# Optimization experiments

Measured on AMD Instinct MI355X. Metric: run time of the kernel, lower is better.

Reference implementation:

```python
import jax, jax.numpy as jnp
import numpy as np

B, S, HID = 1, 4096, 2048
H, KV, D = 16, 8, 128
EPS = 1e-6
ROPE_THETA = 10000.0


def _rms_norm(x, w, eps=EPS):
    # x: [..., D], normalize over last dim in fp32 like Qwen3 RMSNorm
    xf = x.astype(jnp.float32)
    var = jnp.mean(xf * xf, axis=-1, keepdims=True)
    return (xf * jax.lax.rsqrt(var + eps)).astype(x.dtype) * w


def _rotate_half(x):
    x1, x2 = jnp.split(x, 2, axis=-1)
    return jnp.concatenate([-x2, x1], axis=-1)


def setup_inputs() -> dict:
    key = jax.random.key(0)
    ks = jax.random.split(key, 6)
    hidden_states = jax.random.normal(ks[0], (B, S, HID), dtype=jnp.float32)
    wq = jax.random.normal(ks[1], (H * D, HID), dtype=jnp.float32) * 0.02
    wk = jax.random.normal(ks[2], (KV * D, HID), dtype=jnp.float32) * 0.02
    wv = jax.random.normal(ks[3], (KV * D, HID), dtype=jnp.float32) * 0.02
    wo = jax.random.normal(ks[4], (HID, H * D), dtype=jnp.float32) * 0.02
    q_norm_w = jnp.ones((D,), dtype=jnp.float32)
    k_norm_w = jnp.ones((D,), dtype=jnp.float32)
    # real rotary tables: inv_freq over half dim, duplicated (HF convention)
    inv_freq = 1.0 / (ROPE_THETA ** (jnp.arange(0, D, 2, dtype=jnp.float32) / D))
    pos = jnp.arange(S, dtype=jnp.float32)
    freqs = pos[:, None] * inv_freq[None, :]          # [S, D/2]
    emb = jnp.concatenate([freqs, freqs], axis=-1)    # [S, D]
    cos = jnp.cos(emb)[None].astype(jnp.float32)      # [B, S, D]
    sin = jnp.sin(emb)[None].astype(jnp.float32)
    return {"hidden_states": hidden_states, "cos": cos, "sin": sin,
            "wq": wq, "wk": wk, "wv": wv, "wo": wo,
            "q_norm_w": q_norm_w, "k_norm_w": k_norm_w}


def reference(hidden_states, cos, sin, wq, wk, wv, wo, q_norm_w, k_norm_w):
    b, s, _ = hidden_states.shape
    scaling = D ** -0.5
    # QKV projections (no bias), reshape to heads, QK RMSNorm, then [b, h, s, d]
    q = _rms_norm(jnp.einsum('bsh,oh->bso', hidden_states, wq).reshape(b, s, H, D), q_norm_w)
    k = _rms_norm(jnp.einsum('bsh,oh->bso', hidden_states, wk).reshape(b, s, KV, D), k_norm_w)
    v = jnp.einsum('bsh,oh->bso', hidden_states, wv).reshape(b, s, KV, D)
    q = q.transpose(0, 2, 1, 3)  # [b, H, s, d]
    k = k.transpose(0, 2, 1, 3)  # [b, KV, s, d]
    v = v.transpose(0, 2, 1, 3)
    # RoPE (cos/sin broadcast over head dim)
    c = cos[:, None, :, :]
    sn = sin[:, None, :, :]
    q = q * c + _rotate_half(q) * sn
    k = k * c + _rotate_half(k) * sn
    # GQA: repeat KV heads to H
    groups = H // KV
    k = jnp.repeat(k, groups, axis=1)
    v = jnp.repeat(v, groups, axis=1)
    # eager causal attention, softmax in fp32
    scores = jnp.einsum('bhqd,bhkd->bhqk', q, k) * scaling
    causal = jnp.tril(jnp.ones((s, s), dtype=bool))
    scores = jnp.where(causal[None, None], scores, jnp.finfo(jnp.float32).min)
    attn = jax.nn.softmax(scores.astype(jnp.float32), axis=-1).astype(q.dtype)
    out = jnp.einsum('bhqk,bhkd->bhqd', attn, v)
    out = out.transpose(0, 2, 1, 3).reshape(b, s, H * D)
    return jnp.einsum('bso,ho->bsh', out, wo)
```

## Files before the change

### kernel.cpp

```cpp
#include <hip/hip_runtime.h>
#include <hip/hip_bf16.h>

typedef __hip_bfloat16 bf16;
typedef __attribute__((ext_vector_type(8))) short short8;
typedef __attribute__((ext_vector_type(4))) float f32x4;

#define S_LEN 4096
#define HID_DIM 2048

#define QSCALE ((float)(0.08838834764831845 * 1.4426950408889634))

__device__ __forceinline__ void gld_lds16(const void* g, void* l) {
  __builtin_amdgcn_global_load_lds(
      (const __attribute__((address_space(1))) void*)g,
      (__attribute__((address_space(3))) void*)l, 16, 0, 0);
}

__device__ __forceinline__ float fexp2(float x) {
  return __builtin_amdgcn_exp2f(x);
}

__device__ __forceinline__ unsigned cvtpk_bf16(float lo, float hi) {
  unsigned r;
  asm("v_cvt_pk_bf16_f32 %0, %1, %2" : "=v"(r) : "v"(lo), "v"(hi));
  return r;
}

__global__ __launch_bounds__(256) void k_cvt(const float* __restrict__ src,
                                             bf16* __restrict__ dst, int n) {
  long i = ((long)blockIdx.x * 256 + threadIdx.x) * 8;
  if (i >= n) return;
  float4 a = *reinterpret_cast<const float4*>(src + i);
  float4 b = *reinterpret_cast<const float4*>(src + i + 4);
  float v[8] = {a.x, a.y, a.z, a.w, b.x, b.y, b.z, b.w};
  short8 o;
#pragma unroll
  for (int j = 0; j < 8; ++j) {
    bf16 h = __float2bfloat16(v[j]);
    o[j] = *reinterpret_cast<short*>(&h);
  }
  *reinterpret_cast<short8*>(dst + i) = o;
}

template <typename OutT>
__global__ __launch_bounds__(512, 1) void k_gemm256(
    const bf16* __restrict__ A, const bf16* __restrict__ B,
    OutT* __restrict__ C, int M, int N, int K) {
  __shared__ bf16 Al[2][256 * 64];
  __shared__ bf16 Bl[2][256 * 64];
  const int tid = threadIdx.x;
  const int lane = tid & 63;
  const int wid = tid >> 6;
  const int wr = wid >> 2;
  const int wc = wid & 3;
  const long brow = (long)blockIdx.y * 256;
  const long bcol = (long)blockIdx.x * 256;
  const int NT = K >> 6;

  auto stage = [&](int kt, int buf) {
    const bf16* At = A + brow * K + kt * 64;
    const bf16* Bt = B + bcol * K + kt * 64;
#pragma unroll
    for (int i = 0; i < 4; ++i) {
      const int ch = tid + i * 512;
      const int row = ch >> 3;
      const int j = (ch & 7) ^ (row & 7);
      gld_lds16(At + (size_t)row * K + j * 8, &Al[buf][(wid * 64 + i * 512) * 8]);
    }
#pragma unroll
    for (int i = 0; i < 4; ++i) {
      const int ch = tid + i * 512;
      const int row = ch >> 3;
      const int j = (ch & 7) ^ (row & 7);
      gld_lds16(Bt + (size_t)row * K + j * 8, &Bl[buf][(wid * 64 + i * 512) * 8]);
    }
  };

  f32x4 acc0[4][4], acc1[4][4];
#pragma unroll
  for (int m = 0; m < 4; ++m)
#pragma unroll
    for (int n = 0; n < 4; ++n) {
      acc0[m][n] = (f32x4){0.f, 0.f, 0.f, 0.f};
      acc1[m][n] = (f32x4){0.f, 0.f, 0.f, 0.f};
    }

  const int l15 = lane & 15;
  const int cp0 = ((lane >> 4) ^ (lane & 7)) * 8;
  const int cp1 = ((4 + (lane >> 4)) ^ (lane & 7)) * 8;

  stage(0, 0);
  stage(1, 1);
  asm volatile("s_waitcnt vmcnt(8)" ::: "memory");
  __builtin_amdgcn_s_barrier();

  for (int kt = 0; kt < NT; ++kt) {
    const bf16* Ab = &Al[kt & 1][0];
    const bf16* Bb = &Bl[kt & 1][0];
    short8 bB[4][2], aA[4][2];
#pragma unroll
    for (int n = 0; n < 4; ++n) {
      const int rb = (wc * 64 + n * 16 + l15) * 64;
      bB[n][0] = *reinterpret_cast<const short8*>(&Bb[rb + cp0]);
      bB[n][1] = *reinterpret_cast<const short8*>(&Bb[rb + cp1]);
    }
#pragma unroll
    for (int m = 0; m < 4; ++m) {
      const int ra = (wr * 128 + m * 16 + l15) * 64;
      aA[m][0] = *reinterpret_cast<const short8*>(&Ab[ra + cp0]);
      aA[m][1] = *reinterpret_cast<const short8*>(&Ab[ra + cp1]);
    }
    __builtin_amdgcn_s_setprio(1);
#pragma unroll
    for (int m = 0; m < 4; ++m)
#pragma unroll
      for (int n = 0; n < 4; ++n) {
        acc0[m][n] = __builtin_amdgcn_mfma_f32_16x16x32_bf16(aA[m][0], bB[n][0],
                                                             acc0[m][n], 0, 0, 0);
        acc0[m][n] = __builtin_amdgcn_mfma_f32_16x16x32_bf16(aA[m][1], bB[n][1],
                                                             acc0[m][n], 0, 0, 0);
      }
    __builtin_amdgcn_s_setprio(0);
#pragma unroll
    for (int m = 0; m < 4; ++m) {
      const int ra = (wr * 128 + 64 + m * 16 + l15) * 64;
      aA[m][0] = *reinterpret_cast<const short8*>(&Ab[ra + cp0]);
      aA[m][1] = *reinterpret_cast<const short8*>(&Ab[ra + cp1]);
    }
    __builtin_amdgcn_s_setprio(1);
#pragma unroll
    for (int m = 0; m < 4; ++m)
#pragma unroll
      for (int n = 0; n < 4; ++n) {
        acc1[m][n] = __builtin_amdgcn_mfma_f32_16x16x32_bf16(aA[m][0], bB[n][0],
                                                             acc1[m][n], 0, 0, 0);
        acc1[m][n] = __builtin_amdgcn_mfma_f32_16x16x32_bf16(aA[m][1], bB[n][1],
                                                             acc1[m][n], 0, 0, 0);
      }
    __builtin_amdgcn_s_setprio(0);

    if (kt + 1 < NT) {
      __builtin_amdgcn_s_barrier();
      if (kt + 2 < NT) {
        stage(kt + 2, kt & 1);
        asm volatile("s_waitcnt vmcnt(8)" ::: "memory");
      } else {
        asm volatile("s_waitcnt vmcnt(0)" ::: "memory");
      }
      __builtin_amdgcn_s_barrier();
    }
  }

#pragma unroll
  for (int mh = 0; mh < 2; ++mh) {
#pragma unroll
    for (int m = 0; m < 4; ++m) {
      const long r0 = brow + wr * 128 + mh * 64 + m * 16 + (lane >> 4) * 4;
#pragma unroll
      for (int n = 0; n < 4; ++n) {
        const long c0 = bcol + wc * 64 + n * 16 + l15;
        const f32x4 v = mh ? acc1[m][n] : acc0[m][n];
#pragma unroll
        for (int r = 0; r < 4; ++r) {
          if constexpr (sizeof(OutT) == 2)
            C[(r0 + r) * N + c0] = __float2bfloat16(v[r]);
          else
            C[(r0 + r) * N + c0] = v[r];
        }
      }
    }
  }
}

template <typename OutT>
__global__ __launch_bounds__(256) void k_gemm_bt(
    const bf16* __restrict__ A, const bf16* __restrict__ B,
    OutT* __restrict__ C, int M, int N, int K) {
  __shared__ bf16 Al[2][128 * 32];
  __shared__ bf16 Bl[2][128 * 32];
  const int tid = threadIdx.x;
  const int lane = tid & 63;
  const int wid = tid >> 6;
  const int wr = wid >> 1;
  const int wc = wid & 1;
  const long brow = (long)blockIdx.y * 128;
  const long bcol = (long)blockIdx.x * 128;
  const int rsub = lane >> 2;
  const int ksub = (lane & 3) * 8;

  f32x4 acc[4][4];
#pragma unroll
  for (int i = 0; i < 4; ++i)
#pragma unroll
    for (int j = 0; j < 4; ++j) acc[i][j] = (f32x4){0.f, 0.f, 0.f, 0.f};

  const int NT = K >> 5;

  auto stage = [&](int buf, int kt) {
    const long k0 = (long)kt << 5;
#pragma unroll
    for (int ci = 0; ci < 2; ++ci) {
      const int c = wid + ci * 4;
      gld_lds16(A + (brow + c * 16 + rsub) * K + k0 + ksub, &Al[buf][c * 512]);
      gld_lds16(B + (bcol + c * 16 + rsub) * K + k0 + ksub, &Bl[buf][c * 512]);
    }
  };

  stage(0, 0);
  __syncthreads();

  const int arow = wr * 64 + (lane & 15);
  const int nrow = wc * 64 + (lane & 15);
  const int kk = (lane >> 4) * 8;

  for (int t = 0; t < NT; ++t) {
    const int buf = t & 1;
    if (t + 1 < NT) stage(buf ^ 1, t + 1);
    short8 af[4], bfr[4];
#pragma unroll
    for (int mt = 0; mt < 4; ++mt)
      af[mt] = *reinterpret_cast<const short8*>(&Al[buf][(arow + mt * 16) * 32 + kk]);
#pragma unroll
    for (int nt = 0; nt < 4; ++nt)
      bfr[nt] = *reinterpret_cast<const short8*>(&Bl[buf][(nrow + nt * 16) * 32 + kk]);
#pragma unroll
    for (int mt = 0; mt < 4; ++mt)
#pragma unroll
      for (int nt = 0; nt < 4; ++nt)
        acc[mt][nt] = __builtin_amdgcn_mfma_f32_16x16x32_bf16(af[mt], bfr[nt],
                                                              acc[mt][nt], 0, 0, 0);
    __syncthreads();
  }

#pragma unroll
  for (int mt = 0; mt < 4; ++mt) {
    const long r0 = brow + wr * 64 + mt * 16 + (lane >> 4) * 4;
#pragma unroll
    for (int nt = 0; nt < 4; ++nt) {
      const long c0 = bcol + wc * 64 + nt * 16 + (lane & 15);
#pragma unroll
      for (int r = 0; r < 4; ++r) {
        if constexpr (sizeof(OutT) == 2)
          C[(r0 + r) * N + c0] = __float2bfloat16(acc[mt][nt][r]);
        else
          C[(r0 + r) * N + c0] = acc[mt][nt][r];
      }
    }
  }
}

__global__ __launch_bounds__(256) void k_normrope(
    const bf16* __restrict__ QKVb, const float* __restrict__ cosb,
    const float* __restrict__ sinb, const float* __restrict__ qw,
    const float* __restrict__ kw, bf16* __restrict__ Qb, bf16* __restrict__ Kb,
    bf16* __restrict__ Vb) {
  const int lane = threadIdx.x & 63;
  const int row = blockIdx.x * 4 + (threadIdx.x >> 6);
  const int s = row >> 5;
  const int idx = row & 31;
  const bf16* src = QKVb + (size_t)s * 4096 + idx * 128;
  float x0 = __bfloat162float(src[lane]);
  float x1 = __bfloat162float(src[lane + 64]);
  if (idx < 24) {
    float ss = x0 * x0 + x1 * x1;
#pragma unroll
    for (int off = 1; off < 64; off <<= 1) ss += __shfl_xor(ss, off);
    const float rn = rsqrtf(ss * (1.f / 128.f) + 1e-6f);
    const float* w = (idx < 16) ? qw : kw;
    x0 = x0 * rn * w[lane];
    x1 = x1 * rn * w[lane + 64];
    const float c0 = cosb[(size_t)s * 128 + lane];
    const float c1 = cosb[(size_t)s * 128 + lane + 64];
    const float s0 = sinb[(size_t)s * 128 + lane];
    const float s1 = sinb[(size_t)s * 128 + lane + 64];
    float o0 = x0 * c0 - x1 * s0;
    float o1 = x1 * c1 + x0 * s1;
    if (idx < 16) { o0 *= QSCALE; o1 *= QSCALE; }
    bf16* dst = (idx < 16) ? (Qb + ((size_t)idx * S_LEN + s) * 128)
                           : (Kb + ((size_t)(idx - 16) * S_LEN + s) * 128);
    dst[lane] = __float2bfloat16(o0);
    dst[lane + 64] = __float2bfloat16(o1);
  } else {
    bf16* dst = Vb + ((size_t)(idx - 24) * S_LEN + s) * 128;
    dst[lane] = __float2bfloat16(x0);
    dst[lane + 64] = __float2bfloat16(x1);
  }
}

__global__ __launch_bounds__(256) void k_vt(const bf16* __restrict__ Vb,
                                            bf16* __restrict__ Vt) {
  __shared__ bf16 Lds[64][136];
  const int tid = threadIdx.x;
  const int s0 = blockIdx.x * 64;
  const int kv = blockIdx.y;
#pragma unroll
  for (int pass = 0; pass < 4; ++pass) {
    const int c = tid + pass * 256;
    const int r = c >> 4;
    const int off = (c & 15) * 8;
    *reinterpret_cast<short8*>(&Lds[r][off]) =
        *reinterpret_cast<const short8*>(
            &Vb[((size_t)kv * S_LEN + s0 + r) * 128 + off]);
  }
  __syncthreads();
#pragma unroll
  for (int pass = 0; pass < 4; ++pass) {
    const int c = tid + pass * 256;
    const int d = c >> 3;
    const int so = (c & 7) * 8;
    short8 o;
#pragma unroll
    for (int j = 0; j < 8; ++j) {
      bf16 e = Lds[so + j][d];
      o[j] = *reinterpret_cast<short*>(&e);
    }
    *reinterpret_cast<short8*>(&Vt[((size_t)kv * 128 + d) * S_LEN + s0 + so]) = o;
  }
}

__global__ __launch_bounds__(256) void k_attn(const bf16* __restrict__ Qb,
                                              const bf16* __restrict__ Kb,
                                              const bf16* __restrict__ Vt_g,
                                              bf16* __restrict__ AO) {
  __shared__ bf16 Kl[2][64 * 128];
  __shared__ bf16 Vl[2][128 * 64];
  __shared__ bf16 Pl[4][16 * 64];
  const int tid = threadIdx.x;
  const int lane = tid & 63;
  const int wv = tid >> 6;
  const int h = blockIdx.y;
  const int kvh = h >> 1;
  const int c16 = lane & 15;
  const int hi = lane >> 4;
  const int kk = hi * 8;

  const bf16* Kbase = Kb + (size_t)kvh * S_LEN * 128;
  const bf16* Vbase = Vt_g + (size_t)kvh * 128 * S_LEN;

  auto stage = [&](int t, int buf) {
    const bf16* Kt = Kbase + (size_t)t * 64 * 128;
    const bf16* Vt = Vbase + t * 64;
#pragma unroll
    for (int p = 0; p < 4; ++p) {
      const int ch = tid + p * 256;
      const int row = ch >> 4, cp = ch & 15;
      const int c = (cp & 8) | ((cp & 7) ^ (row & 7));
      gld_lds16(Kt + row * 128 + c * 8, &Kl[buf][(wv * 64 + p * 256) * 8]);
    }
#pragma unroll
    for (int p = 0; p < 4; ++p) {
      const int ch = tid + p * 256;
      const int d = ch >> 3, cp = ch & 7;
      const int c = cp ^ (d & 7);
      gld_lds16(Vt + (size_t)d * S_LEN + c * 8, &Vl[buf][(wv * 64 + p * 256) * 8]);
    }
  };

  for (int half = 0; half < 2; ++half) {
    const int qt = half ? (63 - blockIdx.x) : blockIdx.x;
    const int qrow = qt * 64 + wv * 16;
    const int grow = qrow + c16;

    __syncthreads();
    stage(0, 0);

    short8 qf[4];
    {
      const bf16* qp = Qb + ((size_t)h * S_LEN + qrow + c16) * 128 + kk;
#pragma unroll
      for (int ks = 0; ks < 4; ++ks)
        qf[ks] = *reinterpret_cast<const short8*>(qp + ks * 32);
    }

    f32x4 oacc[8];
#pragma unroll
    for (int i = 0; i < 8; ++i) oacc[i] = (f32x4){0.f, 0.f, 0.f, 0.f};
    float m_run = -1e30f;
    float l_part = 0.f;

    auto tile = [&](int t, int buf, bool mask) {
      f32x4 sacc[4];
#pragma unroll
      for (int nt = 0; nt < 4; ++nt) sacc[nt] = (f32x4){0.f, 0.f, 0.f, 0.f};
#pragma unroll
      for (int ks = 0; ks < 4; ++ks) {
#pragma unroll
        for (int nt = 0; nt < 4; ++nt) {
          const int row = nt * 16 + c16;
          const int ck = ks * 4 + hi;
          const int ckp = (ck & 8) | ((ck & 7) ^ (row & 7));
          short8 kf =
              *reinterpret_cast<const short8*>(&Kl[buf][row * 128 + ckp * 8]);
          sacc[nt] = __builtin_amdgcn_mfma_f32_16x16x32_bf16(kf, qf[ks],
                                                             sacc[nt], 0, 0, 0);
        }
      }

      float tm = -1e30f;
#pragma unroll
      for (int nt = 0; nt < 4; ++nt)
#pragma unroll
        for (int r = 0; r < 4; ++r) {
          float sv = sacc[nt][r];
          if (mask && (t * 64 + nt * 16 + 4 * hi + r > grow)) sv = -1e30f;
          sacc[nt][r] = sv;
          tm = fmaxf(tm, sv);
        }
      tm = fmaxf(tm, __shfl_xor(tm, 16));
      tm = fmaxf(tm, __shfl_xor(tm, 32));
      if (__any(tm > m_run + 8.f)) {
        const float mn = fmaxf(m_run, tm);
        const float alpha = fexp2(m_run - mn);
        m_run = mn;
        l_part *= alpha;
#pragma unroll
        for (int dn = 0; dn < 8; ++dn) oacc[dn] *= alpha;
      }

#pragma unroll
      for (int nt = 0; nt < 4; ++nt) {
        const float p0 = fexp2(sacc[nt][0] - m_run);
        const float p1 = fexp2(sacc[nt][1] - m_run);
        const float p2 = fexp2(sacc[nt][2] - m_run);
        const float p3 = fexp2(sacc[nt][3] - m_run);
        l_part += (p0 + p1) + (p2 + p3);
        const unsigned w0 = cvtpk_bf16(p0, p1);
        const unsigned w1 = cvtpk_bf16(p2, p3);
        const int chunk = (2 * nt + (hi >> 1)) ^ (c16 & 7);
        const int base = c16 * 64 + chunk * 8 + 4 * (hi & 1);
        *reinterpret_cast<unsigned*>(&Pl[wv][base]) = w0;
        *reinterpret_cast<unsigned*>(&Pl[wv][base + 2]) = w1;
      }

#pragma unroll
      for (int ks = 0; ks < 2; ++ks) {
        const int pc = (ks * 4 + hi) ^ (c16 & 7);
        short8 pf =
            *reinterpret_cast<const short8*>(&Pl[wv][c16 * 64 + pc * 8]);
#pragma unroll
        for (int dn = 0; dn < 8; ++dn) {
          const int d = dn * 16 + c16;
          const int cvp = (ks * 4 + hi) ^ (d & 7);
          short8 vf =
              *reinterpret_cast<const short8*>(&Vl[buf][d * 64 + cvp * 8]);
          oacc[dn] =
              __builtin_amdgcn_mfma_f32_16x16x32_bf16(vf, pf, oacc[dn], 0, 0, 0);
        }
      }
    };

    __syncthreads();
    int cur = 0;
    for (int t = 0; t < qt; ++t) {
      stage(t + 1, cur ^ 1);
      tile(t, cur, false);
      __syncthreads();
      cur ^= 1;
    }
    tile(qt, cur, true);

    float lt = l_part;
    lt += __shfl_xor(lt, 16);
    lt += __shfl_xor(lt, 32);
    const float inv = 1.f / lt;
    bf16* dst = AO + (size_t)grow * HID_DIM + h * 128;
#pragma unroll
    for (int dn = 0; dn < 8; ++dn) {
#pragma unroll
      for (int w = 0; w < 2; ++w) {
        const unsigned pk = cvtpk_bf16(oacc[dn][2 * w] * inv,
                                       oacc[dn][2 * w + 1] * inv);
        *reinterpret_cast<unsigned*>(&dst[dn * 16 + 4 * hi + 2 * w]) = pk;
      }
    }
  }
}

extern "C" void kernel_launch(void* const* d_in, const int* in_sizes, int n_in,
                              void* d_out, int out_size, void* d_ws,
                              size_t ws_size, hipStream_t stream) {
  (void)in_sizes; (void)n_in; (void)out_size; (void)ws_size;
  const float* hs = (const float*)d_in[0];
  const float* cosb = (const float*)d_in[1];
  const float* sinb = (const float*)d_in[2];
  const float* wq = (const float*)d_in[3];
  const float* wk = (const float*)d_in[4];
  const float* wv = (const float*)d_in[5];
  const float* wo = (const float*)d_in[6];
  const float* qnw = (const float*)d_in[7];
  const float* knw = (const float*)d_in[8];
  float* out = (float*)d_out;
  char* ws = (char*)d_ws;

  bf16* Ah = (bf16*)(ws + 0);
  bf16* Wqkv = (bf16*)(ws + 16777216);
  bf16* Wo = (bf16*)(ws + 33554432);
  bf16* QKVb = (bf16*)(ws + 41943040);
  bf16* Qb = (bf16*)(ws + 75497472);
  bf16* Kb = (bf16*)(ws + 92274688);
  bf16* Vb = (bf16*)(ws + 100663296);
  bf16* AO = (bf16*)(ws + 109051904);
  bf16* Vt = (bf16*)(ws + 125829120);

  auto cvt = [&](const float* s, bf16* d, long n) {
    k_cvt<<<dim3((unsigned)((n / 8 + 255) / 256)), dim3(256), 0, stream>>>(
        s, d, (int)n);
  };
  cvt(hs, Ah, (long)S_LEN * HID_DIM);
  cvt(wq, Wqkv, (long)2048 * 2048);
  cvt(wk, Wqkv + (long)2048 * 2048, (long)1024 * 2048);
  cvt(wv, Wqkv + (long)3072 * 2048, (long)1024 * 2048);
  cvt(wo, Wo, (long)2048 * 2048);

  k_gemm256<bf16><<<dim3(16, 16), dim3(512), 0, stream>>>(Ah, Wqkv, QKVb, 4096,
                                                          4096, 2048);
  k_normrope<<<dim3(32768), dim3(256), 0, stream>>>(QKVb, cosb, sinb, qnw, knw,
                                                    Qb, Kb, Vb);
  k_vt<<<dim3(64, 8), dim3(256), 0, stream>>>(Vb, Vt);
  k_attn<<<dim3(32, 16), dim3(256), 0, stream>>>(Qb, Kb, Vt, AO);
  k_gemm_bt<float><<<dim3(16, 32), dim3(256), 0, stream>>>(AO, Wo, out, 4096,
                                                           2048, 2048);
}
```

Baseline: 287.9 us.

## Split causal attention KV range across two blocks and merge fp32 partials

The attention kernel now has each wave handle two 16-row query groups (128 query rows per block), so every K/V fragment read from LDS feeds twice as many MFMAs. The causal KV range for each 128-row group is split between two blocks, keeping the same grid size with balanced work. Each block writes unnormalized fp32 output partials plus row max and sum to workspace, and a new merge kernel combines them into bf16. The trade-off is extra register pressure, an additional launch, and roughly 64MB of fp32 partials written and read back. Workspace buffers are re-laid out so the partials reuse regions freed by earlier stages.

```diff
diff --git a/kernel.cpp b/kernel.cpp
--- a/kernel.cpp
+++ b/kernel.cpp
@@ -318,18 +318,20 @@
   }
 }
 
-__global__ __launch_bounds__(256) void k_attn(const bf16* __restrict__ Qb,
-                                              const bf16* __restrict__ Kb,
-                                              const bf16* __restrict__ Vt_g,
-                                              bf16* __restrict__ AO) {
+__global__ __launch_bounds__(256) void k_attn_part(
+    const bf16* __restrict__ Qb, const bf16* __restrict__ Kb,
+    const bf16* __restrict__ Vt_g, float* __restrict__ Opart,
+    float* __restrict__ ML) {
   __shared__ bf16 Kl[2][64 * 128];
   __shared__ bf16 Vl[2][128 * 64];
-  __shared__ bf16 Pl[4][16 * 64];
+  __shared__ bf16 Pl[4][32 * 64];
   const int tid = threadIdx.x;
   const int lane = tid & 63;
   const int wv = tid >> 6;
   const int h = blockIdx.y;
   const int kvh = h >> 1;
+  const int pr = blockIdx.x >> 1;
+  const int part = blockIdx.x & 1;
   const int c16 = lane & 15;
   const int hi = lane >> 4;
   const int kk = hi * 8;
@@ -356,32 +358,48 @@
     }
   };
 
-  for (int half = 0; half < 2; ++half) {
-    const int qt = half ? (63 - blockIdx.x) : blockIdx.x;
-    const int qrow = qt * 64 + wv * 16;
-    const int grow = qrow + c16;
-
-    __syncthreads();
-    stage(0, 0);
-
-    short8 qf[4];
+  for (int hf = 0; hf < 2; ++hf) {
+    const int g = hf ? (31 - pr) : pr;
+    const int qrowA = g * 128 + wv * 16;
+    const int growA = qrowA + c16;
+    const int growB = growA + 64;
+    const int t0 = part ? (g + 1) : 0;
+    const int t1 = part ? (2 * g + 2) : (g + 1);
+    const int diagA = 2 * g;
+    const int diagB = 2 * g + 1;
+
+    if (hf) __syncthreads();
+    stage(t0, 0);
+
+    short8 qfA[4], qfB[4];
     {
-      const bf16* qp = Qb + ((size_t)h * S_LEN + qrow + c16) * 128 + kk;
-#pragma unroll
-      for (int ks = 0; ks < 4; ++ks)
-        qf[ks] = *reinterpret_cast<const short8*>(qp + ks * 32);
-    }
-
-    f32x4 oacc[8];
-#pragma unroll
-    for (int i = 0; i < 8; ++i) oacc[i] = (f32x4){0.f, 0.f, 0.f, 0.f};
-    float m_run = -1e30f;
-    float l_part = 0.f;
-
-    auto tile = [&](int t, int buf, bool mask) {
-      f32x4 sacc[4];
-#pragma unroll
-      for (int nt = 0; nt < 4; ++nt) sacc[nt] = (f32x4){0.f, 0.f, 0.f, 0.f};
+      const bf16* qpA = Qb + ((size_t)h * S_LEN + growA) * 128 + kk;
+      const bf16* qpB = Qb + ((size_t)h * S_LEN + growB) * 128 + kk;
+#pragma unroll
+      for (int ks = 0; ks < 4; ++ks) {
+        qfA[ks] = *reinterpret_cast<const short8*>(qpA + ks * 32);
+        qfB[ks] = *reinterpret_cast<const short8*>(qpB + ks * 32);
+      }
+    }
+
+    f32x4 oA[8], oB[8];
+#pragma unroll
+    for (int i = 0; i < 8; ++i) {
+      oA[i] = (f32x4){0.f, 0.f, 0.f, 0.f};
+      oB[i] = (f32x4){0.f, 0.f, 0.f, 0.f};
+    }
+    float mA = -1e30f, mB = -1e30f, lA = 0.f, lB = 0.f;
+
+    auto tile = [&](int t, int buf) {
+      const bool doA = (t <= diagA);
+      const bool mkA = (t == diagA);
+      const bool mkB = (t == diagB);
+      f32x4 sA[4], sB[4];
+#pragma unroll
+      for (int nt = 0; nt < 4; ++nt) {
+        sA[nt] = (f32x4){0.f, 0.f, 0.f, 0.f};
+        sB[nt] = (f32x4){0.f, 0.f, 0.f, 0.f};
+      }
 #pragma unroll
       for (int ks = 0; ks < 4; ++ks) {
 #pragma unroll
@@ -391,89 +409,169 @@
           const int ckp = (ck & 8) | ((ck & 7) ^ (row & 7));
           short8 kf =
               *reinterpret_cast<const short8*>(&Kl[buf][row * 128 + ckp * 8]);
-          sacc[nt] = __builtin_amdgcn_mfma_f32_16x16x32_bf16(kf, qf[ks],
-                                                             sacc[nt], 0, 0, 0);
+          if (doA)
+            sA[nt] = __builtin_amdgcn_mfma_f32_16x16x32_bf16(kf, qfA[ks],
+                                                             sA[nt], 0, 0, 0);
+          sB[nt] = __builtin_amdgcn_mfma_f32_16x16x32_bf16(kf, qfB[ks],
+                                                           sB[nt], 0, 0, 0);
         }
       }
 
-      float tm = -1e30f;
-#pragma unroll
-      for (int nt = 0; nt < 4; ++nt)
-#pragma unroll
-        for (int r = 0; r < 4; ++r) {
-          float sv = sacc[nt][r];
-          if (mask && (t * 64 + nt * 16 + 4 * hi + r > grow)) sv = -1e30f;
-          sacc[nt][r] = sv;
-          tm = fmaxf(tm, sv);
+      if (doA) {
+        float tm = -1e30f;
+#pragma unroll
+        for (int nt = 0; nt < 4; ++nt)
+#pragma unroll
+          for (int r = 0; r < 4; ++r) {
+            float sv = sA[nt][r];
+            if (mkA && (t * 64 + nt * 16 + 4 * hi + r > growA)) sv = -1e30f;
+            sA[nt][r] = sv;
+            tm = fmaxf(tm, sv);
+          }
+        tm = fmaxf(tm, __shfl_xor(tm, 16));
+        tm = fmaxf(tm, __shfl_xor(tm, 32));
+        if (__any(tm > mA + 8.f)) {
+          const float mn = fmaxf(mA, tm);
+          const float alpha = fexp2(mA - mn);
+          mA = mn;
+          lA *= alpha;
+#pragma unroll
+          for (int dn = 0; dn < 8; ++dn) oA[dn] *= alpha;
         }
-      tm = fmaxf(tm, __shfl_xor(tm, 16));
-      tm = fmaxf(tm, __shfl_xor(tm, 32));
-      if (__any(tm > m_run + 8.f)) {
-        const float mn = fmaxf(m_run, tm);
-        const float alpha = fexp2(m_run - mn);
-        m_run = mn;
-        l_part *= alpha;
-#pragma unroll
-        for (int dn = 0; dn < 8; ++dn) oacc[dn] *= alpha;
-      }
-
-#pragma unroll
-      for (int nt = 0; nt < 4; ++nt) {
-        const float p0 = fexp2(sacc[nt][0] - m_run);
-        const float p1 = fexp2(sacc[nt][1] - m_run);
-        const float p2 = fexp2(sacc[nt][2] - m_run);
-        const float p3 = fexp2(sacc[nt][3] - m_run);
-        l_part += (p0 + p1) + (p2 + p3);
-        const unsigned w0 = cvtpk_bf16(p0, p1);
-        const unsigned w1 = cvtpk_bf16(p2, p3);
-        const int chunk = (2 * nt + (hi >> 1)) ^ (c16 & 7);
-        const int base = c16 * 64 + chunk * 8 + 4 * (hi & 1);
-        *reinterpret_cast<unsigned*>(&Pl[wv][base]) = w0;
-        *reinterpret_cast<unsigned*>(&Pl[wv][base + 2]) = w1;
+#pragma unroll
+        for (int nt = 0; nt < 4; ++nt) {
+          const float p0 = fexp2(sA[nt][0] - mA);
+          const float p1 = fexp2(sA[nt][1] - mA);
+          const float p2 = fexp2(sA[nt][2] - mA);
+          const float p3 = fexp2(sA[nt][3] - mA);
+          lA += (p0 + p1) + (p2 + p3);
+          const unsigned w0 = cvtpk_bf16(p0, p1);
+          const unsigned w1 = cvtpk_bf16(p2, p3);
+          const int chunk = (2 * nt + (hi >> 1)) ^ (c16 & 7);
+          const int base = c16 * 64 + chunk * 8 + 4 * (hi & 1);
+          *reinterpret_cast<unsigned*>(&Pl[wv][base]) = w0;
+          *reinterpret_cast<unsigned*>(&Pl[wv][base + 2]) = w1;
+        }
+      }
+      {
+        float tm = -1e30f;
+#pragma unroll
+        for (int nt = 0; nt < 4; ++nt)
+#pragma unroll
+          for (int r = 0; r < 4; ++r) {
+            float sv = sB[nt][r];
+            if (mkB && (t * 64 + nt * 16 + 4 * hi + r > growB)) sv = -1e30f;
+            sB[nt][r] = sv;
+            tm = fmaxf(tm, sv);
+          }
+        tm = fmaxf(tm, __shfl_xor(tm, 16));
+        tm = fmaxf(tm, __shfl_xor(tm, 32));
+        if (__any(tm > mB + 8.f)) {
+          const float mn = fmaxf(mB, tm);
+          const float alpha = fexp2(mB - mn);
+          mB = mn;
+          lB *= alpha;
+#pragma unroll
+          for (int dn = 0; dn < 8; ++dn) oB[dn] *= alpha;
+        }
+#pragma unroll
+        for (int nt = 0; nt < 4; ++nt) {
+          const float p0 = fexp2(sB[nt][0] - mB);
+          const float p1 = fexp2(sB[nt][1] - mB);
+          const float p2 = fexp2(sB[nt][2] - mB);
+          const float p3 = fexp2(sB[nt][3] - mB);
+          lB += (p0 + p1) + (p2 + p3);
+          const unsigned w0 = cvtpk_bf16(p0, p1);
+          const unsigned w1 = cvtpk_bf16(p2, p3);
+          const int chunk = (2 * nt + (hi >> 1)) ^ (c16 & 7);
+          const int base = (16 + c16) * 64 + chunk * 8 + 4 * (hi & 1);
+          *reinterpret_cast<unsigned*>(&Pl[wv][base]) = w0;
+          *reinterpret_cast<unsigned*>(&Pl[wv][base + 2]) = w1;
+        }
       }
 
 #pragma unroll
       for (int ks = 0; ks < 2; ++ks) {
         const int pc = (ks * 4 + hi) ^ (c16 & 7);
-        short8 pf =
-            *reinterpret_cast<const short8*>(&Pl[wv][c16 * 64 + pc * 8]);
+        short8 pfA;
+        if (doA)
+          pfA = *reinterpret_cast<const short8*>(&Pl[wv][c16 * 64 + pc * 8]);
+        short8 pfB =
+            *reinterpret_cast<const short8*>(&Pl[wv][(16 + c16) * 64 + pc * 8]);
 #pragma unroll
         for (int dn = 0; dn < 8; ++dn) {
           const int d = dn * 16 + c16;
           const int cvp = (ks * 4 + hi) ^ (d & 7);
           short8 vf =
               *reinterpret_cast<const short8*>(&Vl[buf][d * 64 + cvp * 8]);
-          oacc[dn] =
-              __builtin_amdgcn_mfma_f32_16x16x32_bf16(vf, pf, oacc[dn], 0, 0, 0);
+          if (doA)
+            oA[dn] = __builtin_amdgcn_mfma_f32_16x16x32_bf16(vf, pfA, oA[dn],
+                                                             0, 0, 0);
+          oB[dn] = __builtin_amdgcn_mfma_f32_16x16x32_bf16(vf, pfB, oB[dn],
+                                                           0, 0, 0);
         }
       }
     };
 
     __syncthreads();
     int cur = 0;
-    for (int t = 0; t < qt; ++t) {
+    for (int t = t0; t < t1 - 1; ++t) {
       stage(t + 1, cur ^ 1);
-      tile(t, cur, false);
+      tile(t, cur);
       __syncthreads();
       cur ^= 1;
     }
-    tile(qt, cur, true);
-
-    float lt = l_part;
-    lt += __shfl_xor(lt, 16);
-    lt += __shfl_xor(lt, 32);
-    const float inv = 1.f / lt;
-    bf16* dst = AO + (size_t)grow * HID_DIM + h * 128;
+    tile(t1 - 1, cur);
+
+    float ltA = lA, ltB = lB;
+    ltA += __shfl_xor(ltA, 16);
+    ltA += __shfl_xor(ltA, 32);
+    ltB += __shfl_xor(ltB, 16);
+    ltB += __shfl_xor(ltB, 32);
+    const int job = (h * 32 + g) * 2 + part;
+    float* Op = Opart + (size_t)job * 128 * 128;
+    float* MLp = ML + (size_t)job * 256;
+    const int rA = wv * 16 + c16;
+    const int rB = rA + 64;
 #pragma unroll
     for (int dn = 0; dn < 8; ++dn) {
-#pragma unroll
-      for (int w = 0; w < 2; ++w) {
-        const unsigned pk = cvtpk_bf16(oacc[dn][2 * w] * inv,
-                                       oacc[dn][2 * w + 1] * inv);
-        *reinterpret_cast<unsigned*>(&dst[dn * 16 + 4 * hi + 2 * w]) = pk;
-      }
-    }
-  }
+      *reinterpret_cast<float4*>(&Op[rA * 128 + dn * 16 + 4 * hi]) =
+          *reinterpret_cast<float4*>(&oA[dn]);
+      *reinterpret_cast<float4*>(&Op[rB * 128 + dn * 16 + 4 * hi]) =
+          *reinterpret_cast<float4*>(&oB[dn]);
+    }
+    if (lane < 16) {
+      MLp[rA] = mA;
+      MLp[128 + rA] = ltA;
+      MLp[rB] = mB;
+      MLp[128 + rB] = ltB;
+    }
+  }
+}
+
+__global__ __launch_bounds__(256) void k_merge(const float* __restrict__ Opart,
+                                               const float* __restrict__ ML,
+                                               bf16* __restrict__ AO) {
+  const int idx = blockIdx.x * 4 + (threadIdx.x >> 6);
+  const int lane = threadIdx.x & 63;
+  const int h = idx >> 12;
+  const int s = idx & 4095;
+  const int g = s >> 7, rowin = s & 127;
+  const int j0 = (h * 32 + g) * 2;
+  const float m0 = ML[(size_t)j0 * 256 + rowin];
+  const float l0 = ML[(size_t)j0 * 256 + 128 + rowin];
+  const float m1 = ML[(size_t)(j0 + 1) * 256 + rowin];
+  const float l1 = ML[(size_t)(j0 + 1) * 256 + 128 + rowin];
+  const float mm = fmaxf(m0, m1);
+  const float a0 = fexp2(m0 - mm), a1 = fexp2(m1 - mm);
+  const float inv = 1.f / (l0 * a0 + l1 * a1);
+  const float2 o0 = *reinterpret_cast<const float2*>(
+      &Opart[((size_t)j0 * 128 + rowin) * 128 + lane * 2]);
+  const float2 o1 = *reinterpret_cast<const float2*>(
+      &Opart[((size_t)(j0 + 1) * 128 + rowin) * 128 + lane * 2]);
+  bf16* dst = AO + (size_t)s * HID_DIM + h * 128 + lane * 2;
+  dst[0] = __float2bfloat16((o0.x * a0 + o1.x * a1) * inv);
+  dst[1] = __float2bfloat16((o0.y * a0 + o1.y * a1) * inv);
 }
 
 extern "C" void kernel_launch(void* const* d_in, const int* in_sizes, int n_in,
@@ -494,13 +592,15 @@
 
   bf16* Ah = (bf16*)(ws + 0);
   bf16* Wqkv = (bf16*)(ws + 16777216);
-  bf16* Wo = (bf16*)(ws + 33554432);
-  bf16* QKVb = (bf16*)(ws + 41943040);
-  bf16* Qb = (bf16*)(ws + 75497472);
-  bf16* Kb = (bf16*)(ws + 92274688);
-  bf16* Vb = (bf16*)(ws + 100663296);
+  bf16* QKVb = (bf16*)(ws + 33554432);
+  bf16* Qb = (bf16*)(ws + 67108864);
+  bf16* Kb = (bf16*)(ws + 83886080);
+  bf16* Vb = (bf16*)(ws + 92274688);
+  bf16* Vt = (bf16*)(ws + 100663296);
   bf16* AO = (bf16*)(ws + 109051904);
-  bf16* Vt = (bf16*)(ws + 125829120);
+  bf16* Wo = (bf16*)(ws + 125829120);
+  float* Opart = (float*)(ws + 0);
+  float* ML = (float*)(ws + 92274688);
 
   auto cvt = [&](const float* s, bf16* d, long n) {
     k_cvt<<<dim3((unsigned)((n / 8 + 255) / 256)), dim3(256), 0, stream>>>(
@@ -517,7 +617,8 @@
   k_normrope<<<dim3(32768), dim3(256), 0, stream>>>(QKVb, cosb, sinb, qnw, knw,
                                                     Qb, Kb, Vb);
   k_vt<<<dim3(64, 8), dim3(256), 0, stream>>>(Vb, Vt);
-  k_attn<<<dim3(32, 16), dim3(256), 0, stream>>>(Qb, Kb, Vt, AO);
+  k_attn_part<<<dim3(32, 16), dim3(256), 0, stream>>>(Qb, Kb, Vt, Opart, ML);
+  k_merge<<<dim3(16384), dim3(256), 0, stream>>>(Opart, ML, AO);
   k_gemm_bt<float><<<dim3(16, 32), dim3(256), 0, stream>>>(AO, Wo, out, 4096,
                                                            2048, 2048);
 }
```

Result: slower. 383.8 us (+33.3%).

## Read V fragments directly from global in MFMA-ready layout, one q-tile per block

Applied to the files above, without the earlier changes.

The V transpose kernel now writes V in a chunked layout ([s/8][d][8]) so each lane's MFMA operand is one contiguous 16-byte global load. The attention kernel drops V staging in LDS and loads V fragments straight from global/L2, which halves the LDS footprint and the staging traffic. It also replaces the paired causal q-tile loop with one q-tile per block on a grid twice as large. The risks are global-load latency inside the inner PV loop, with no prefetch, and load imbalance now that heavy and light causal tiles are no longer paired per block.

```diff
diff --git a/kernel.cpp b/kernel.cpp
--- a/kernel.cpp
+++ b/kernel.cpp
@@ -288,7 +288,7 @@
 }
 
 __global__ __launch_bounds__(256) void k_vt(const bf16* __restrict__ Vb,
-                                            bf16* __restrict__ Vt) {
+                                            bf16* __restrict__ Vg) {
   __shared__ bf16 Lds[64][136];
   const int tid = threadIdx.x;
   const int s0 = blockIdx.x * 64;
@@ -306,24 +306,25 @@
 #pragma unroll
   for (int pass = 0; pass < 4; ++pass) {
     const int c = tid + pass * 256;
-    const int d = c >> 3;
-    const int so = (c & 7) * 8;
+    const int ck = c >> 7;
+    const int d = c & 127;
     short8 o;
 #pragma unroll
     for (int j = 0; j < 8; ++j) {
-      bf16 e = Lds[so + j][d];
+      bf16 e = Lds[ck * 8 + j][d];
       o[j] = *reinterpret_cast<short*>(&e);
     }
-    *reinterpret_cast<short8*>(&Vt[((size_t)kv * 128 + d) * S_LEN + s0 + so]) = o;
+    *reinterpret_cast<short8*>(
+        &Vg[(size_t)kv * S_LEN * 128 +
+            ((size_t)(blockIdx.x * 8 + ck) * 128 + d) * 8]) = o;
   }
 }
 
 __global__ __launch_bounds__(256) void k_attn(const bf16* __restrict__ Qb,
                                               const bf16* __restrict__ Kb,
-                                              const bf16* __restrict__ Vt_g,
+                                              const bf16* __restrict__ Vg,
                                               bf16* __restrict__ AO) {
   __shared__ bf16 Kl[2][64 * 128];
-  __shared__ bf16 Vl[2][128 * 64];
   __shared__ bf16 Pl[4][16 * 64];
   const int tid = threadIdx.x;
   const int lane = tid & 63;
@@ -335,11 +336,10 @@
   const int kk = hi * 8;
 
   const bf16* Kbase = Kb + (size_t)kvh * S_LEN * 128;
-  const bf16* Vbase = Vt_g + (size_t)kvh * 128 * S_LEN;
+  const bf16* Vgh = Vg + (size_t)kvh * S_LEN * 128;
 
   auto stage = [&](int t, int buf) {
     const bf16* Kt = Kbase + (size_t)t * 64 * 128;
-    const bf16* Vt = Vbase + t * 64;
 #pragma unroll
     for (int p = 0; p < 4; ++p) {
       const int ch = tid + p * 256;
@@ -347,131 +347,121 @@
       const int c = (cp & 8) | ((cp & 7) ^ (row & 7));
       gld_lds16(Kt + row * 128 + c * 8, &Kl[buf][(wv * 64 + p * 256) * 8]);
     }
-#pragma unroll
-    for (int p = 0; p < 4; ++p) {
-      const int ch = tid + p * 256;
-      const int d = ch >> 3, cp = ch & 7;
-      const int c = cp ^ (d & 7);
-      gld_lds16(Vt + (size_t)d * S_LEN + c * 8, &Vl[buf][(wv * 64 + p * 256) * 8]);
-    }
   };
 
-  for (int half = 0; half < 2; ++half) {
-    const int qt = half ? (63 - blockIdx.x) : blockIdx.x;
-    const int qrow = qt * 64 + wv * 16;
-    const int grow = qrow + c16;
-
+  const int qt = 63 - blockIdx.x;
+  const int qrow = qt * 64 + wv * 16;
+  const int grow = qrow + c16;
+
+  stage(0, 0);
+
+  short8 qf[4];
+  {
+    const bf16* qp = Qb + ((size_t)h * S_LEN + grow) * 128 + kk;
+#pragma unroll
+    for (int ks = 0; ks < 4; ++ks)
+      qf[ks] = *reinterpret_cast<const short8*>(qp + ks * 32);
+  }
+
+  f32x4 oacc[8];
+#pragma unroll
+  for (int i = 0; i < 8; ++i) oacc[i] = (f32x4){0.f, 0.f, 0.f, 0.f};
+  float m_run = -1e30f;
+  float l_part = 0.f;
+
+  auto tile = [&](int t, int buf, bool mask) {
+    f32x4 sacc[4];
+#pragma unroll
+    for (int nt = 0; nt < 4; ++nt) sacc[nt] = (f32x4){0.f, 0.f, 0.f, 0.f};
+#pragma unroll
+    for (int ks = 0; ks < 4; ++ks) {
+#pragma unroll
+      for (int nt = 0; nt < 4; ++nt) {
+        const int row = nt * 16 + c16;
+        const int ck = ks * 4 + hi;
+        const int ckp = (ck & 8) | ((ck & 7) ^ (row & 7));
+        short8 kf =
+            *reinterpret_cast<const short8*>(&Kl[buf][row * 128 + ckp * 8]);
+        sacc[nt] = __builtin_amdgcn_mfma_f32_16x16x32_bf16(kf, qf[ks],
+                                                           sacc[nt], 0, 0, 0);
+      }
+    }
+
+    float tm = -1e30f;
+#pragma unroll
+    for (int nt = 0; nt < 4; ++nt)
+#pragma unroll
+      for (int r = 0; r < 4; ++r) {
+        float sv = sacc[nt][r];
+        if (mask && (t * 64 + nt * 16 + 4 * hi + r > grow)) sv = -1e30f;
+        sacc[nt][r] = sv;
+        tm = fmaxf(tm, sv);
+      }
+    tm = fmaxf(tm, __shfl_xor(tm, 16));
+    tm = fmaxf(tm, __shfl_xor(tm, 32));
+    if (__any(tm > m_run + 8.f)) {
+      const float mn = fmaxf(m_run, tm);
+      const float alpha = fexp2(m_run - mn);
+      m_run = mn;
+      l_part *= alpha;
+#pragma unroll
+      for (int dn = 0; dn < 8; ++dn) oacc[dn] *= alpha;
+    }
+
+#pragma unroll
+    for (int nt = 0; nt < 4; ++nt) {
+      const float p0 = fexp2(sacc[nt][0] - m_run);
+      const float p1 = fexp2(sacc[nt][1] - m_run);
+      const float p2 = fexp2(sacc[nt][2] - m_run);
+      const float p3 = fexp2(sacc[nt][3] - m_run);
+      l_part += (p0 + p1) + (p2 + p3);
+      const unsigned w0 = cvtpk_bf16(p0, p1);
+      const unsigned w1 = cvtpk_bf16(p2, p3);
+      const int chunk = (2 * nt + (hi >> 1)) ^ (c16 & 7);
+      const int base = c16 * 64 + chunk * 8 + 4 * (hi & 1);
+      *reinterpret_cast<unsigned*>(&Pl[wv][base]) = w0;
+      *reinterpret_cast<unsigned*>(&Pl[wv][base + 2]) = w1;
+    }
+
+    const bf16* vt0 = Vgh + (size_t)t * 8192;
+#pragma unroll
+    for (int ks = 0; ks < 2; ++ks) {
+      const int pc = (ks * 4 + hi) ^ (c16 & 7);
+      short8 pf =
+          *reinterpret_cast<const short8*>(&Pl[wv][c16 * 64 + pc * 8]);
+      const bf16* vck = vt0 + (ks * 4 + hi) * 1024;
+#pragma unroll
+      for (int dn = 0; dn < 8; ++dn) {
+        short8 vf = *reinterpret_cast<const short8*>(
+            vck + (dn * 16 + c16) * 8);
+        oacc[dn] =
+            __builtin_amdgcn_mfma_f32_16x16x32_bf16(vf, pf, oacc[dn], 0, 0, 0);
+      }
+    }
+  };
+
+  __syncthreads();
+  int cur = 0;
+  for (int t = 0; t < qt; ++t) {
+    stage(t + 1, cur ^ 1);
+    tile(t, cur, false);
     __syncthreads();
-    stage(0, 0);
-
-    short8 qf[4];
-    {
-      const bf16* qp = Qb + ((size_t)h * S_LEN + qrow + c16) * 128 + kk;
-#pragma unroll
-      for (int ks = 0; ks < 4; ++ks)
-        qf[ks] = *reinterpret_cast<const short8*>(qp + ks * 32);
-    }
-
-    f32x4 oacc[8];
-#pragma unroll
-    for (int i = 0; i < 8; ++i) oacc[i] = (f32x4){0.f, 0.f, 0.f, 0.f};
-    float m_run = -1e30f;
-    float l_part = 0.f;
-
-    auto tile = [&](int t, int buf, bool mask) {
-      f32x4 sacc[4];
-#pragma unroll
-      for (int nt = 0; nt < 4; ++nt) sacc[nt] = (f32x4){0.f, 0.f, 0.f, 0.f};
-#pragma unroll
-      for (int ks = 0; ks < 4; ++ks) {
-#pragma unroll
-        for (int nt = 0; nt < 4; ++nt) {
-          const int row = nt * 16 + c16;
-          const int ck = ks * 4 + hi;
-          const int ckp = (ck & 8) | ((ck & 7) ^ (row & 7));
-          short8 kf =
-              *reinterpret_cast<const short8*>(&Kl[buf][row * 128 + ckp * 8]);
-          sacc[nt] = __builtin_amdgcn_mfma_f32_16x16x32_bf16(kf, qf[ks],
-                                                             sacc[nt], 0, 0, 0);
-        }
-      }
-
-      float tm = -1e30f;
-#pragma unroll
-      for (int nt = 0; nt < 4; ++nt)
-#pragma unroll
-        for (int r = 0; r < 4; ++r) {
-          float sv = sacc[nt][r];
-          if (mask && (t * 64 + nt * 16 + 4 * hi + r > grow)) sv = -1e30f;
-          sacc[nt][r] = sv;
-          tm = fmaxf(tm, sv);
-        }
-      tm = fmaxf(tm, __shfl_xor(tm, 16));
-      tm = fmaxf(tm, __shfl_xor(tm, 32));
-      if (__any(tm > m_run + 8.f)) {
-        const float mn = fmaxf(m_run, tm);
-        const float alpha = fexp2(m_run - mn);
-        m_run = mn;
-        l_part *= alpha;
-#pragma unroll
-        for (int dn = 0; dn < 8; ++dn) oacc[dn] *= alpha;
-      }
-
-#pragma unroll
-      for (int nt = 0; nt < 4; ++nt) {
-        const float p0 = fexp2(sacc[nt][0] - m_run);
-        const float p1 = fexp2(sacc[nt][1] - m_run);
-        const float p2 = fexp2(sacc[nt][2] - m_run);
-        const float p3 = fexp2(sacc[nt][3] - m_run);
-        l_part += (p0 + p1) + (p2 + p3);
-        const unsigned w0 = cvtpk_bf16(p0, p1);
-        const unsigned w1 = cvtpk_bf16(p2, p3);
-        const int chunk = (2 * nt + (hi >> 1)) ^ (c16 & 7);
-        const int base = c16 * 64 + chunk * 8 + 4 * (hi & 1);
-        *reinterpret_cast<unsigned*>(&Pl[wv][base]) = w0;
-        *reinterpret_cast<unsigned*>(&Pl[wv][base + 2]) = w1;
-      }
-
-#pragma unroll
-      for (int ks = 0; ks < 2; ++ks) {
-        const int pc = (ks * 4 + hi) ^ (c16 & 7);
-        short8 pf =
-            *reinterpret_cast<const short8*>(&Pl[wv][c16 * 64 + pc * 8]);
-#pragma unroll
-        for (int dn = 0; dn < 8; ++dn) {
-          const int d = dn * 16 + c16;
-          const int cvp = (ks * 4 + hi) ^ (d & 7);
-          short8 vf =
-              *reinterpret_cast<const short8*>(&Vl[buf][d * 64 + cvp * 8]);
-          oacc[dn] =
-              __builtin_amdgcn_mfma_f32_16x16x32_bf16(vf, pf, oacc[dn], 0, 0, 0);
-        }
-      }
-    };
-
-    __syncthreads();
-    int cur = 0;
-    for (int t = 0; t < qt; ++t) {
-      stage(t + 1, cur ^ 1);
-      tile(t, cur, false);
-      __syncthreads();
-      cur ^= 1;
-    }
-    tile(qt, cur, true);
-
-    float lt = l_part;
-    lt += __shfl_xor(lt, 16);
-    lt += __shfl_xor(lt, 32);
-    const float inv = 1.f / lt;
-    bf16* dst = AO + (size_t)grow * HID_DIM + h * 128;
-#pragma unroll
-    for (int dn = 0; dn < 8; ++dn) {
-#pragma unroll
-      for (int w = 0; w < 2; ++w) {
-        const unsigned pk = cvtpk_bf16(oacc[dn][2 * w] * inv,
-                                       oacc[dn][2 * w + 1] * inv);
-        *reinterpret_cast<unsigned*>(&dst[dn * 16 + 4 * hi + 2 * w]) = pk;
-      }
+    cur ^= 1;
+  }
+  tile(qt, cur, true);
+
+  float lt = l_part;
+  lt += __shfl_xor(lt, 16);
+  lt += __shfl_xor(lt, 32);
+  const float inv = 1.f / lt;
+  bf16* dst = AO + (size_t)grow * HID_DIM + h * 128;
+#pragma unroll
+  for (int dn = 0; dn < 8; ++dn) {
+#pragma unroll
+    for (int w = 0; w < 2; ++w) {
+      const unsigned pk = cvtpk_bf16(oacc[dn][2 * w] * inv,
+                                     oacc[dn][2 * w + 1] * inv);
+      *reinterpret_cast<unsigned*>(&dst[dn * 16 + 4 * hi + 2 * w]) = pk;
     }
   }
 }
@@ -500,7 +490,7 @@
   bf16* Kb = (bf16*)(ws + 92274688);
   bf16* Vb = (bf16*)(ws + 100663296);
   bf16* AO = (bf16*)(ws + 109051904);
-  bf16* Vt = (bf16*)(ws + 125829120);
+  bf16* Vg = (bf16*)(ws + 125829120);
 
   auto cvt = [&](const float* s, bf16* d, long n) {
     k_cvt<<<dim3((unsigned)((n / 8 + 255) / 256)), dim3(256), 0, stream>>>(
@@ -516,8 +506,8 @@
                                                           4096, 2048);
   k_normrope<<<dim3(32768), dim3(256), 0, stream>>>(QKVb, cosb, sinb, qnw, knw,
                                                     Qb, Kb, Vb);
-  k_vt<<<dim3(64, 8), dim3(256), 0, stream>>>(Vb, Vt);
-  k_attn<<<dim3(32, 16), dim3(256), 0, stream>>>(Qb, Kb, Vt, AO);
+  k_vt<<<dim3(64, 8), dim3(256), 0, stream>>>(Vb, Vg);
+  k_attn<<<dim3(64, 16), dim3(256), 0, stream>>>(Qb, Kb, Vg, AO);
   k_gemm_bt<float><<<dim3(16, 32), dim3(256), 0, stream>>>(AO, Wo, out, 4096,
                                                            2048, 2048);
 }
```

Measured after the change: 351.2 us. +22.0%, slower.

## Replace output-projection GEMM with 256x128 tile, BK=64, swizzled LDS pipeline

Applied to the files above, without the earlier changes.

The output projection GEMM moves from 128x128 tiles with K-step 32 and 256 threads to 256x128 tiles with K-step 64 and 512 threads. It adds XOR-swizzled LDS staging, prefetches two stages ahead with explicit vmcnt waits and raw barriers, and raises wave priority around the MFMA block. The aim is more data reuse per tile, fewer bank conflicts and better overlap of loads with compute. The grid shrinks to 256 blocks, which may leave some CUs idle.

```diff
diff --git a/kernel.cpp b/kernel.cpp
--- a/kernel.cpp
+++ b/kernel.cpp
@@ -172,79 +172,102 @@
   }
 }
 
-template <typename OutT>
-__global__ __launch_bounds__(256) void k_gemm_bt(
+__global__ __launch_bounds__(512, 1) void k_gemm_op(
     const bf16* __restrict__ A, const bf16* __restrict__ B,
-    OutT* __restrict__ C, int M, int N, int K) {
-  __shared__ bf16 Al[2][128 * 32];
-  __shared__ bf16 Bl[2][128 * 32];
+    float* __restrict__ C, int M, int N, int K) {
+  __shared__ bf16 Al[2][256 * 64];
+  __shared__ bf16 Bl[2][128 * 64];
   const int tid = threadIdx.x;
   const int lane = tid & 63;
   const int wid = tid >> 6;
   const int wr = wid >> 1;
   const int wc = wid & 1;
-  const long brow = (long)blockIdx.y * 128;
+  const long brow = (long)blockIdx.y * 256;
   const long bcol = (long)blockIdx.x * 128;
-  const int rsub = lane >> 2;
-  const int ksub = (lane & 3) * 8;
+  const int NT = K >> 6;
+
+  auto stage = [&](int kt, int buf) {
+    const bf16* At = A + brow * K + kt * 64;
+    const bf16* Bt = B + bcol * K + kt * 64;
+#pragma unroll
+    for (int i = 0; i < 4; ++i) {
+      const int ch = tid + i * 512;
+      const int row = ch >> 3;
+      const int j = (ch & 7) ^ (row & 7);
+      gld_lds16(At + (size_t)row * K + j * 8, &Al[buf][(wid * 64 + i * 512) * 8]);
+    }
+#pragma unroll
+    for (int i = 0; i < 2; ++i) {
+      const int ch = tid + i * 512;
+      const int row = ch >> 3;
+      const int j = (ch & 7) ^ (row & 7);
+      gld_lds16(Bt + (size_t)row * K + j * 8, &Bl[buf][(wid * 64 + i * 512) * 8]);
+    }
+  };
 
   f32x4 acc[4][4];
 #pragma unroll
-  for (int i = 0; i < 4; ++i)
-#pragma unroll
-    for (int j = 0; j < 4; ++j) acc[i][j] = (f32x4){0.f, 0.f, 0.f, 0.f};
-
-  const int NT = K >> 5;
-
-  auto stage = [&](int buf, int kt) {
-    const long k0 = (long)kt << 5;
-#pragma unroll
-    for (int ci = 0; ci < 2; ++ci) {
-      const int c = wid + ci * 4;
-      gld_lds16(A + (brow + c * 16 + rsub) * K + k0 + ksub, &Al[buf][c * 512]);
-      gld_lds16(B + (bcol + c * 16 + rsub) * K + k0 + ksub, &Bl[buf][c * 512]);
-    }
-  };
+  for (int m = 0; m < 4; ++m)
+#pragma unroll
+    for (int n = 0; n < 4; ++n) acc[m][n] = (f32x4){0.f, 0.f, 0.f, 0.f};
+
+  const int l15 = lane & 15;
+  const int cp0 = ((lane >> 4) ^ (lane & 7)) * 8;
+  const int cp1 = ((4 + (lane >> 4)) ^ (lane & 7)) * 8;
 
   stage(0, 0);
-  __syncthreads();
-
-  const int arow = wr * 64 + (lane & 15);
-  const int nrow = wc * 64 + (lane & 15);
-  const int kk = (lane >> 4) * 8;
-
-  for (int t = 0; t < NT; ++t) {
-    const int buf = t & 1;
-    if (t + 1 < NT) stage(buf ^ 1, t + 1);
-    short8 af[4], bfr[4];
-#pragma unroll
-    for (int mt = 0; mt < 4; ++mt)
-      af[mt] = *reinterpret_cast<const short8*>(&Al[buf][(arow + mt * 16) * 32 + kk]);
-#pragma unroll
-    for (int nt = 0; nt < 4; ++nt)
-      bfr[nt] = *reinterpret_cast<const short8*>(&Bl[buf][(nrow + nt * 16) * 32 + kk]);
-#pragma unroll
-    for (int mt = 0; mt < 4; ++mt)
-#pragma unroll
-      for (int nt = 0; nt < 4; ++nt)
-        acc[mt][nt] = __builtin_amdgcn_mfma_f32_16x16x32_bf16(af[mt], bfr[nt],
-                                                              acc[mt][nt], 0, 0, 0);
-    __syncthreads();
-  }
-
-#pragma unroll
-  for (int mt = 0; mt < 4; ++mt) {
-    const long r0 = brow + wr * 64 + mt * 16 + (lane >> 4) * 4;
-#pragma unroll
-    for (int nt = 0; nt < 4; ++nt) {
-      const long c0 = bcol + wc * 64 + nt * 16 + (lane & 15);
-#pragma unroll
-      for (int r = 0; r < 4; ++r) {
-        if constexpr (sizeof(OutT) == 2)
-          C[(r0 + r) * N + c0] = __float2bfloat16(acc[mt][nt][r]);
-        else
-          C[(r0 + r) * N + c0] = acc[mt][nt][r];
-      }
+  stage(1, 1);
+  asm volatile("s_waitcnt vmcnt(6)" ::: "memory");
+  __builtin_amdgcn_s_barrier();
+
+  for (int kt = 0; kt < NT; ++kt) {
+    const bf16* Ab = &Al[kt & 1][0];
+    const bf16* Bb = &Bl[kt & 1][0];
+    short8 bB[4][2], aA[4][2];
+#pragma unroll
+    for (int n = 0; n < 4; ++n) {
+      const int rb = (wc * 64 + n * 16 + l15) * 64;
+      bB[n][0] = *reinterpret_cast<const short8*>(&Bb[rb + cp0]);
+      bB[n][1] = *reinterpret_cast<const short8*>(&Bb[rb + cp1]);
+    }
+#pragma unroll
+    for (int m = 0; m < 4; ++m) {
+      const int ra = (wr * 64 + m * 16 + l15) * 64;
+      aA[m][0] = *reinterpret_cast<const short8*>(&Ab[ra + cp0]);
+      aA[m][1] = *reinterpret_cast<const short8*>(&Ab[ra + cp1]);
+    }
+    __builtin_amdgcn_s_setprio(1);
+#pragma unroll
+    for (int m = 0; m < 4; ++m)
+#pragma unroll
+      for (int n = 0; n < 4; ++n) {
+        acc[m][n] = __builtin_amdgcn_mfma_f32_16x16x32_bf16(aA[m][0], bB[n][0],
+                                                            acc[m][n], 0, 0, 0);
+        acc[m][n] = __builtin_amdgcn_mfma_f32_16x16x32_bf16(aA[m][1], bB[n][1],
+                                                            acc[m][n], 0, 0, 0);
+      }
+    __builtin_amdgcn_s_setprio(0);
+
+    if (kt + 1 < NT) {
+      __builtin_amdgcn_s_barrier();
+      if (kt + 2 < NT) {
+        stage(kt + 2, kt & 1);
+        asm volatile("s_waitcnt vmcnt(6)" ::: "memory");
+      } else {
+        asm volatile("s_waitcnt vmcnt(0)" ::: "memory");
+      }
+      __builtin_amdgcn_s_barrier();
+    }
+  }
+
+#pragma unroll
+  for (int m = 0; m < 4; ++m) {
+    const long r0 = brow + wr * 64 + m * 16 + (lane >> 4) * 4;
+#pragma unroll
+    for (int n = 0; n < 4; ++n) {
+      const long c0 = bcol + wc * 64 + n * 16 + l15;
+#pragma unroll
+      for (int r = 0; r < 4; ++r) C[(r0 + r) * N + c0] = acc[m][n][r];
     }
   }
 }
@@ -366,7 +389,7 @@
 
     short8 qf[4];
     {
-      const bf16* qp = Qb + ((size_t)h * S_LEN + qrow + c16) * 128 + kk;
+      const bf16* qp = Qb + ((size_t)h * S_LEN + grow) * 128 + kk;
 #pragma unroll
       for (int ks = 0; ks < 4; ++ks)
         qf[ks] = *reinterpret_cast<const short8*>(qp + ks * 32);
@@ -518,6 +541,6 @@
                                                     Qb, Kb, Vb);
   k_vt<<<dim3(64, 8), dim3(256), 0, stream>>>(Vb, Vt);
   k_attn<<<dim3(32, 16), dim3(256), 0, stream>>>(Qb, Kb, Vt, AO);
-  k_gemm_bt<float><<<dim3(16, 32), dim3(256), 0, stream>>>(AO, Wo, out, 4096,
-                                                           2048, 2048);
-}
+  k_gemm_op<<<dim3(16, 16), dim3(512), 0, stream>>>(AO, Wo, out, 4096, 2048,
+                                                    2048);
+}
```

Result: no change. 284.2 us (-1.3%).
